# Optimization experiments

Hardware: AMD Instinct MI355X
Metric: run time of the kernel (lower is better)

The kernel has to match this reference:

```python
import jax, jax.numpy as jnp
import numpy as np

EMBED = 1024
HEADS = 16
HEAD_DIM = EMBED // HEADS
HIDDEN = 4096
EPS = 1e-5


def setup_inputs() -> dict:
    key = jax.random.key(0)
    ks = jax.random.split(key, 16)
    s_e = 1.0 / np.sqrt(EMBED)
    s_h = 1.0 / np.sqrt(HIDDEN)
    return {
        "x": jax.random.normal(ks[0], (8, 1024, EMBED), dtype=jnp.float32),
        "ln1_g": jnp.ones((EMBED,), jnp.float32),
        "ln1_b": jnp.zeros((EMBED,), jnp.float32),
        "ln2_g": jnp.ones((EMBED,), jnp.float32),
        "ln2_b": jnp.zeros((EMBED,), jnp.float32),
        "wq": jax.random.uniform(ks[1], (EMBED, EMBED), jnp.float32, -s_e, s_e),
        "bq": jax.random.uniform(ks[2], (EMBED,), jnp.float32, -s_e, s_e),
        "wk": jax.random.uniform(ks[3], (EMBED, EMBED), jnp.float32, -s_e, s_e),
        "bk": jax.random.uniform(ks[4], (EMBED,), jnp.float32, -s_e, s_e),
        "wv": jax.random.uniform(ks[5], (EMBED, EMBED), jnp.float32, -s_e, s_e),
        "bv": jax.random.uniform(ks[6], (EMBED,), jnp.float32, -s_e, s_e),
        "wo": jax.random.uniform(ks[7], (EMBED, EMBED), jnp.float32, -s_e, s_e),
        "bo": jax.random.uniform(ks[8], (EMBED,), jnp.float32, -s_e, s_e),
        "w1": jax.random.uniform(ks[9], (EMBED, HIDDEN), jnp.float32, -s_e, s_e),
        "b1": jax.random.uniform(ks[10], (HIDDEN,), jnp.float32, -s_e, s_e),
        "w2": jax.random.uniform(ks[11], (HIDDEN, EMBED), jnp.float32, -s_h, s_h),
        "b2": jax.random.uniform(ks[12], (EMBED,), jnp.float32, -s_h, s_h),
    }


def _layernorm(x, g, b):
    mu = jnp.mean(x, axis=-1, keepdims=True)
    var = jnp.mean((x - mu) ** 2, axis=-1, keepdims=True)
    return (x - mu) * jax.lax.rsqrt(var + EPS) * g + b


def reference(x, ln1_g, ln1_b, ln2_g, ln2_b, wq, bq, wk, bk, wv, bv, wo, bo, w1, b1, w2, b2):
    B, N, E = x.shape
    scale = HEAD_DIM ** (-0.5)
    # --- attention sublayer (pre-norm) ---
    h = _layernorm(x, ln1_g, ln1_b)
    q = (h @ wq + bq).reshape(B, N, HEADS, HEAD_DIM).transpose(0, 2, 1, 3) * scale
    k = (h @ wk + bk).reshape(B, N, HEADS, HEAD_DIM).transpose(0, 2, 1, 3)
    v = (h @ wv + bv).reshape(B, N, HEADS, HEAD_DIM).transpose(0, 2, 1, 3)
    scores = jnp.einsum("bhqd,bhkd->bhqk", q, k)
    attn = jax.nn.softmax(scores, axis=-1)
    ctx = jnp.einsum("bhqk,bhkd->bhqd", attn, v)
    ctx = ctx.transpose(0, 2, 1, 3).reshape(B, N, E)
    x = x + (ctx @ wo + bo)
    # --- FFN sublayer (pre-norm) ---
    h2 = _layernorm(x, ln2_g, ln2_b)
    ff = jax.nn.relu(h2 @ w1 + b1) @ w2 + b2
    return x + ff
```

## Files before the change

kernel.cpp:

```cpp
#include <hip/hip_runtime.h>
#include <hip/hip_bf16.h>

typedef __attribute__((ext_vector_type(4))) float f32x4;
typedef __attribute__((ext_vector_type(16))) float f32x16;
typedef __attribute__((ext_vector_type(8))) __bf16 bf16x8;
typedef __attribute__((ext_vector_type(4))) __bf16 bf16x4;
typedef __attribute__((ext_vector_type(4))) unsigned int u32x4;

static constexpr int E    = 1024;
static constexpr int TOK  = 8192;
static constexpr int HID  = 4096;

#define DEVINL __device__ __forceinline__

DEVINL void gload16(const void* g, void* l) {
  __builtin_amdgcn_global_load_lds((__attribute__((address_space(1))) void*)g,
                                   (__attribute__((address_space(3))) void*)l, 16, 0, 0);
}

#define ABAR()  asm volatile("s_barrier" ::: "memory")
#define AVM(n)  asm volatile("s_waitcnt vmcnt(" #n ")" ::: "memory")
#define CVTPK(dst, lo, hi) asm("v_cvt_pk_bf16_f32 %0, %1, %2" : "=v"(dst) : "v"(lo), "v"(hi))
#define PLSWAP(a, b) asm("v_permlane32_swap_b32 %0, %1" : "+v"(a), "+v"(b))

__global__ __launch_bounds__(256) void wconv_kernel(const float* __restrict__ W,
                                                    __bf16* __restrict__ Wt,
                                                    int K, int N) {
  __shared__ float tile[32][33];
  const int t  = threadIdx.x;
  const long k0 = (long)blockIdx.y * 32;
  const long n0 = (long)blockIdx.x * 32;
  const int r  = t >> 3;
  const int c4 = (t & 7) * 4;
  float4 v = *(const float4*)&W[(k0 + r) * N + n0 + c4];
  tile[r][c4 + 0] = v.x; tile[r][c4 + 1] = v.y;
  tile[r][c4 + 2] = v.z; tile[r][c4 + 3] = v.w;
  __syncthreads();
  bf16x4 o;
#pragma unroll
  for (int i = 0; i < 4; ++i) o[i] = (__bf16)tile[c4 + i][r];
  *(bf16x4*)&Wt[(n0 + r) * K + k0 + c4] = o;
}

__global__ __launch_bounds__(256) void ln_kernel(const float* __restrict__ X,
                                                 const float* __restrict__ g,
                                                 const float* __restrict__ be,
                                                 __bf16* __restrict__ O) {
  const int t = threadIdx.x;
  const long row = blockIdx.x;
  float4 v = *(const float4*)&X[row * E + t * 4];
  float s  = v.x + v.y + v.z + v.w;
  float ss = v.x * v.x + v.y * v.y + v.z * v.z + v.w * v.w;
#pragma unroll
  for (int off = 32; off; off >>= 1) {
    s  += __shfl_down(s, off);
    ss += __shfl_down(ss, off);
  }
  __shared__ float red[8];
  const int w = t >> 6;
  if ((t & 63) == 0) { red[w] = s; red[4 + w] = ss; }
  __syncthreads();
  s  = red[0] + red[1] + red[2] + red[3];
  ss = red[4] + red[5] + red[6] + red[7];
  const float mean = s * (1.0f / E);
  const float var  = ss * (1.0f / E) - mean * mean;
  const float rstd = rsqrtf(var + 1e-5f);
  float4 gv = *(const float4*)&g[t * 4];
  float4 bv = *(const float4*)&be[t * 4];
  bf16x4 o;
  o[0] = (__bf16)((v.x - mean) * rstd * gv.x + bv.x);
  o[1] = (__bf16)((v.y - mean) * rstd * gv.y + bv.y);
  o[2] = (__bf16)((v.z - mean) * rstd * gv.z + bv.z);
  o[3] = (__bf16)((v.w - mean) * rstd * gv.w + bv.w);
  *(bf16x4*)&O[row * E + t * 4] = o;
}

template <bool RELU, bool RESID, bool OUTBF, int NB>
__global__ __launch_bounds__(512, 2) void gemm8_kernel(const __bf16* __restrict__ A,
                                                       const __bf16* __restrict__ Bt,
                                                       const float* __restrict__ bias0,
                                                       const float* __restrict__ bias1,
                                                       const float* __restrict__ bias2,
                                                       const float* resid,
                                                       void* Cout,
                                                       int M, int N, int K) {
  extern __shared__ char lds[];
  const int tid  = threadIdx.x;
  const int lane = tid & 63;
  const int l15  = lane & 15;
  const int wid  = tid >> 6;
  const int wr   = wid >> 2;
  const int wc   = wid & 3;

  const int nwg  = gridDim.x * gridDim.y;
  const int flat = blockIdx.x + gridDim.x * blockIdx.y;
  const int swz  = (flat & 7) * (nwg >> 3) + (flat >> 3);
  const int bx   = swz % gridDim.x;
  const int by   = swz / gridDim.x;
  const long brow = (long)by * 256;
  const long bcol = (long)bx * 128;

  const __bf16* Ab = A  + brow * K;
  const __bf16* Bb = Bt + bcol * K;
  const int NT = K >> 6;

  char* bA0 = lds;
  char* bA1 = lds + 49152;
  char* bA2 = lds + 98304;

  auto stageA = [&](int k0, char* base, int seg0, int seg1) {
    {
      const int r = seg0 + (tid >> 3);
      const int p = (tid & 7) ^ (r & 7);
      gload16(Ab + (long)r * K + k0 + p * 8, base + seg0 * 128 + tid * 16);
    }
    {
      const int r = seg1 + (tid >> 3);
      const int p = (tid & 7) ^ (r & 7);
      gload16(Ab + (long)r * K + k0 + p * 8, base + seg1 * 128 + tid * 16);
    }
  };
  auto stageB = [&](int k0, char* base) {
#pragma unroll
    for (int i = 0; i < 2; ++i) {
      const int c = i * 64 + (tid >> 3);
      const int p = (tid & 7) ^ (c & 7);
      gload16(Bb + (long)c * K + k0 + p * 8, base + 32768 + i * 8192 + tid * 16);
    }
  };

  f32x4 acc[8][2];
  const f32x4 z4 = {0.f, 0.f, 0.f, 0.f};
#pragma unroll
  for (int m = 0; m < 8; ++m) { acc[m][0] = z4; acc[m][1] = z4; }

  stageA(0, bA0, 0, 128);
  stageA(0, bA0, 64, 192);
  stageB(0, bA0);
  stageA(64, bA1, 0, 128);
  stageA(64, bA1, 64, 192);
  stageB(64, bA1);
  AVM(6);
  ABAR();

  for (int t = 0; t < NT; ++t) {
    const int k2 = (t + 2 < NT) ? ((t + 2) << 6) : 0;

    bf16x8 af[4][2], bfr[2][2];
#pragma unroll
    for (int m = 0; m < 4; ++m)
#pragma unroll
      for (int kk = 0; kk < 2; ++kk) {
        const int row = wr * 128 + m * 16 + l15;
        const int p   = ((kk << 2) + (lane >> 4)) ^ (row & 7);
        af[m][kk] = *(const bf16x8*)(bA0 + row * 128 + p * 16);
      }
#pragma unroll
    for (int n = 0; n < 2; ++n)
#pragma unroll
      for (int kk = 0; kk < 2; ++kk) {
        const int col = wc * 32 + n * 16 + l15;
        const int p   = ((kk << 2) + (lane >> 4)) ^ (col & 7);
        bfr[n][kk] = *(const bf16x8*)(bA0 + 32768 + col * 128 + p * 16);
      }
    stageA(k2, bA2, 0, 128);
    stageB(k2, bA2);
    ABAR();
    __builtin_amdgcn_s_setprio(1);
#pragma unroll
    for (int m = 0; m < 4; ++m)
#pragma unroll
      for (int n = 0; n < 2; ++n) {
        acc[m][n] = __builtin_amdgcn_mfma_f32_16x16x32_bf16(af[m][0], bfr[n][0], acc[m][n], 0, 0, 0);
        acc[m][n] = __builtin_amdgcn_mfma_f32_16x16x32_bf16(af[m][1], bfr[n][1], acc[m][n], 0, 0, 0);
      }
    __builtin_amdgcn_s_setprio(0);
    ABAR();

#pragma unroll
    for (int m = 0; m < 4; ++m)
#pragma unroll
      for (int kk = 0; kk < 2; ++kk) {
        const int row = wr * 128 + (m + 4) * 16 + l15;
        const int p   = ((kk << 2) + (lane >> 4)) ^ (row & 7);
        af[m][kk] = *(const bf16x8*)(bA0 + row * 128 + p * 16);
      }
    stageA(k2, bA2, 64, 192);
    ABAR();
    __builtin_amdgcn_s_setprio(1);
#pragma unroll
    for (int m = 0; m < 4; ++m)
#pragma unroll
      for (int n = 0; n < 2; ++n) {
        acc[m + 4][n] = __builtin_amdgcn_mfma_f32_16x16x32_bf16(af[m][0], bfr[n][0], acc[m + 4][n], 0, 0, 0);
        acc[m + 4][n] = __builtin_amdgcn_mfma_f32_16x16x32_bf16(af[m][1], bfr[n][1], acc[m + 4][n], 0, 0, 0);
      }
    __builtin_amdgcn_s_setprio(0);
    AVM(6);
    ABAR();

    char* tmp = bA0; bA0 = bA1; bA1 = bA2; bA2 = tmp;
  }
  AVM(0);

#pragma unroll
  for (int m = 0; m < 8; ++m) {
#pragma unroll
    for (int n = 0; n < 2; ++n) {
      const long col = bcol + wc * 32 + n * 16 + l15;
      float bb;
      if (NB == 3) {
        const float* bp = (col < 1024) ? bias0 : ((col < 2048) ? bias1 : bias2);
        bb = bp[col & 1023];
      } else {
        bb = bias0[col];
      }
#pragma unroll
      for (int j = 0; j < 4; ++j) {
        const long row = brow + wr * 128 + m * 16 + (lane >> 4) * 4 + j;
        float val = acc[m][n][j] + bb;
        if (RELU) val = fmaxf(val, 0.f);
        const long idx = row * N + col;
        if (RESID) val += resid[idx];
        if (OUTBF) ((__bf16*)Cout)[idx] = (__bf16)val;
        else       ((float*)Cout)[idx]  = val;
      }
    }
  }
}

__global__ __launch_bounds__(256, 3) void attn_kernel(const __bf16* __restrict__ QKV,
                                                      __bf16* __restrict__ Og) {
  __shared__ __align__(16) __bf16 Qs[128 * 64];
  __shared__ __align__(16) __bf16 Ks[2][64 * 64];
  __shared__ __align__(16) __bf16 Vt[2][64 * 64];

  const int QSTR = 3072;
  const int t    = threadIdx.x;
  const int lane = t & 63;
  const int w    = t >> 6;
  const int l31  = lane & 31;
  const int h    = lane >> 5;
  const int b    = blockIdx.y >> 4;
  const int hh   = blockIdx.y & 15;
  const long row0 = (long)b * 1024 + (long)blockIdx.x * 128;
  const long kvrow0 = (long)b * 1024;
  const int colQ = hh * 64;
  const int colK = colQ + 1024;
  const int colV = colQ + 2048;

#pragma unroll
  for (int j = 0; j < 4; ++j) {
    const int c = j * 256 + t;
    const int r = c >> 3;
    const int p = (c & 7) ^ (r & 7);
    gload16(QKV + (row0 + r) * QSTR + colQ + p * 8, (char*)Qs + c * 16);
  }
#pragma unroll
  for (int j = 0; j < 2; ++j) {
    const int c = j * 256 + t;
    const int r = c >> 3;
    const int p = (c & 7) ^ (r & 7);
    gload16(QKV + (kvrow0 + r) * QSTR + colK + p * 8, (char*)Ks[0] + c * 16);
  }
  bf16x8 vv[2];
#pragma unroll
  for (int j = 0; j < 2; ++j) {
    const int c = j * 256 + t;
    const int key = c >> 3, dc = c & 7;
    vv[j] = *(const bf16x8*)(QKV + (kvrow0 + key) * QSTR + colV + dc * 8);
  }
  AVM(0);
#pragma unroll
  for (int j = 0; j < 2; ++j) {
    const int c = j * 256 + t;
    const int key = c >> 3, dc = c & 7;
#pragma unroll
    for (int e = 0; e < 8; ++e) {
      const int d = dc * 8 + e;
      *(__bf16*)((char*)Vt[0] + d * 128 + (((key >> 3) ^ dc) * 16) + (key & 7) * 2) = vv[j][e];
    }
  }
  __syncthreads();

  bf16x8 bq[4];
  {
    const int qrow = w * 32 + l31;
#pragma unroll
    for (int kk = 0; kk < 4; ++kk) {
      const int p = (kk * 2 + h) ^ (qrow & 7);
      bq[kk] = *(const bf16x8*)((const char*)Qs + qrow * 128 + p * 16);
    }
  }

  f32x16 ctx0, ctx1;
#pragma unroll
  for (int r = 0; r < 16; ++r) { ctx0[r] = 0.f; ctx1[r] = 0.f; }
  float m = -INFINITY, l = 0.f;

  for (int kb = 0; kb < 16; ++kb) {
    const int cur = kb & 1, nxt = cur ^ 1;
    const int kb1 = (kb + 1 < 16) ? kb + 1 : kb;
    const long kr1 = kvrow0 + kb1 * 64;

#pragma unroll
    for (int j = 0; j < 2; ++j) {
      const int c = j * 256 + t;
      const int key = c >> 3, dc = c & 7;
      vv[j] = *(const bf16x8*)(QKV + (kr1 + key) * QSTR + colV + dc * 8);
    }
#pragma unroll
    for (int j = 0; j < 2; ++j) {
      const int c = j * 256 + t;
      const int r = c >> 3;
      const int p = (c & 7) ^ (r & 7);
      gload16(QKV + (kr1 + r) * QSTR + colK + p * 8, (char*)Ks[nxt] + c * 16);
    }

    f32x16 s0, s1;
#pragma unroll
    for (int r = 0; r < 16; ++r) { s0[r] = 0.f; s1[r] = 0.f; }
    __builtin_amdgcn_s_setprio(1);
#pragma unroll
    for (int kk = 0; kk < 4; ++kk) {
      const int pce = kk * 2 + h;
      const int p0i = pce ^ (l31 & 7);
      bf16x8 ak0 = *(const bf16x8*)((const char*)Ks[cur] + l31 * 128 + p0i * 16);
      bf16x8 ak1 = *(const bf16x8*)((const char*)Ks[cur] + (32 + l31) * 128 + p0i * 16);
      s0 = __builtin_amdgcn_mfma_f32_32x32x16_bf16(ak0, bq[kk], s0, 0, 0, 0);
      s1 = __builtin_amdgcn_mfma_f32_32x32x16_bf16(ak1, bq[kk], s1, 0, 0, 0);
    }
    __builtin_amdgcn_s_setprio(0);

    float mx = s0[0];
#pragma unroll
    for (int r = 1; r < 16; ++r) mx = fmaxf(mx, s0[r]);
#pragma unroll
    for (int r = 0; r < 16; ++r) mx = fmaxf(mx, s1[r]);
    mx = fmaxf(mx, __shfl_xor(mx, 32));

    if (!__all(mx - m <= 64.f)) {
      const float mn = fmaxf(m, mx);
      const float corr = __expf((m - mn) * 0.125f);
      l *= corr;
#pragma unroll
      for (int r = 0; r < 16; ++r) { ctx0[r] *= corr; ctx1[r] *= corr; }
      m = mn;
    }
    f32x16 p0, p1;
    float rs = 0.f;
#pragma unroll
    for (int r = 0; r < 16; ++r) { p0[r] = __expf((s0[r] - m) * 0.125f); rs += p0[r]; }
#pragma unroll
    for (int r = 0; r < 16; ++r) { p1[r] = __expf((s1[r] - m) * 0.125f); rs += p1[r]; }
    rs += __shfl_xor(rs, 32);
    l += rs;

    AVM(2);
#pragma unroll
    for (int j = 0; j < 2; ++j) {
      const int c = j * 256 + t;
      const int key = c >> 3, dc = c & 7;
#pragma unroll
      for (int e = 0; e < 8; ++e) {
        const int d = dc * 8 + e;
        *(__bf16*)((char*)Vt[nxt] + d * 128 + (((key >> 3) ^ dc) * 16) + (key & 7) * 2) = vv[j][e];
      }
    }

    bf16x8 paf[4];
#pragma unroll
    for (int ks = 0; ks < 4; ++ks) {
      const int base = (ks & 1) * 8;
      unsigned a0, a1, b0, b1;
      if (ks < 2) {
        CVTPK(a0, p0[base + 0], p0[base + 1]);
        CVTPK(b0, p0[base + 4], p0[base + 5]);
        CVTPK(a1, p0[base + 2], p0[base + 3]);
        CVTPK(b1, p0[base + 6], p0[base + 7]);
      } else {
        CVTPK(a0, p1[base + 0], p1[base + 1]);
        CVTPK(b0, p1[base + 4], p1[base + 5]);
        CVTPK(a1, p1[base + 2], p1[base + 3]);
        CVTPK(b1, p1[base + 6], p1[base + 7]);
      }
      PLSWAP(a0, b0);
      PLSWAP(a1, b1);
      u32x4 wv4; wv4[0] = a0; wv4[1] = a1; wv4[2] = b0; wv4[3] = b1;
      paf[ks] = __builtin_bit_cast(bf16x8, wv4);
    }

    __builtin_amdgcn_s_setprio(1);
#pragma unroll
    for (int ks = 0; ks < 4; ++ks) {
      const int pce = ks * 2 + h;
      bf16x8 av0 = *(const bf16x8*)((const char*)Vt[cur] + l31 * 128 + ((pce ^ (l31 >> 3)) * 16));
      bf16x8 av1 = *(const bf16x8*)((const char*)Vt[cur] + (32 + l31) * 128 + ((pce ^ (4 + (l31 >> 3))) * 16));
      ctx0 = __builtin_amdgcn_mfma_f32_32x32x16_bf16(av0, paf[ks], ctx0, 0, 0, 0);
      ctx1 = __builtin_amdgcn_mfma_f32_32x32x16_bf16(av1, paf[ks], ctx1, 0, 0, 0);
    }
    __builtin_amdgcn_s_setprio(0);

    __syncthreads();
  }

  const float inv = 1.0f / l;
  const long orow = row0 + w * 32 + l31;
#pragma unroll
  for (int f = 0; f < 2; ++f)
#pragma unroll
    for (int tq = 0; tq < 4; ++tq) {
      bf16x4 o;
#pragma unroll
      for (int e = 0; e < 4; ++e) {
        const float v = (f ? ctx1[tq * 4 + e] : ctx0[tq * 4 + e]) * inv;
        o[e] = (__bf16)v;
      }
      const int col = colQ + f * 32 + tq * 8 + h * 4;
      *(bf16x4*)&Og[orow * E + col] = o;
    }
}

extern "C" void kernel_launch(void* const* d_in, const int* in_sizes, int n_in,
                              void* d_out, int out_size, void* d_ws, size_t ws_size,
                              hipStream_t stream) {
  const float* x     = (const float*)d_in[0];
  const float* ln1g  = (const float*)d_in[1];
  const float* ln1b  = (const float*)d_in[2];
  const float* ln2g  = (const float*)d_in[3];
  const float* ln2b  = (const float*)d_in[4];
  const float* wq    = (const float*)d_in[5];
  const float* bq    = (const float*)d_in[6];
  const float* wk    = (const float*)d_in[7];
  const float* bk    = (const float*)d_in[8];
  const float* wv    = (const float*)d_in[9];
  const float* bv    = (const float*)d_in[10];
  const float* wo    = (const float*)d_in[11];
  const float* bo    = (const float*)d_in[12];
  const float* w1    = (const float*)d_in[13];
  const float* b1    = (const float*)d_in[14];
  const float* w2    = (const float*)d_in[15];
  const float* b2    = (const float*)d_in[16];
  float* out = (float*)d_out;

  char* ws = (char*)d_ws;
  const size_t MB = 1024 * 1024;
  __bf16* Wqkv = (__bf16*)(ws + 0 * MB);
  __bf16* Wot  = (__bf16*)(ws + 6 * MB);
  __bf16* W1t  = (__bf16*)(ws + 8 * MB);
  __bf16* W2t  = (__bf16*)(ws + 16 * MB);
  __bf16* h    = (__bf16*)(ws + 24 * MB);
  __bf16* qkv  = (__bf16*)(ws + 40 * MB);
  __bf16* ctx  = (__bf16*)(ws + 88 * MB);
  __bf16* ff1  = (__bf16*)(ws + 40 * MB);

  const dim3 blk(256);
  const dim3 blk512(512);
  const size_t GLDS = 147456;

  wconv_kernel<<<dim3(E / 32, E / 32), blk, 0, stream>>>(wq, Wqkv, E, E);
  wconv_kernel<<<dim3(E / 32, E / 32), blk, 0, stream>>>(wk, Wqkv + 1024 * 1024, E, E);
  wconv_kernel<<<dim3(E / 32, E / 32), blk, 0, stream>>>(wv, Wqkv + 2048 * 1024, E, E);
  wconv_kernel<<<dim3(E / 32, E / 32), blk, 0, stream>>>(wo, Wot, E, E);
  wconv_kernel<<<dim3(HID / 32, E / 32), blk, 0, stream>>>(w1, W1t, E, HID);
  wconv_kernel<<<dim3(E / 32, HID / 32), blk, 0, stream>>>(w2, W2t, HID, E);

  ln_kernel<<<TOK, blk, 0, stream>>>(x, ln1g, ln1b, h);

  gemm8_kernel<false, false, true, 3><<<dim3(3072 / 128, TOK / 256), blk512, GLDS, stream>>>(
      h, Wqkv, bq, bk, bv, nullptr, qkv, TOK, 3072, E);

  attn_kernel<<<dim3(8, 128), blk, 0, stream>>>(qkv, ctx);

  gemm8_kernel<false, true, false, 1><<<dim3(E / 128, TOK / 256), blk512, GLDS, stream>>>(
      ctx, Wot, bo, nullptr, nullptr, x, out, TOK, E, E);

  ln_kernel<<<TOK, blk, 0, stream>>>(out, ln2g, ln2b, h);

  gemm8_kernel<true, false, true, 1><<<dim3(HID / 128, TOK / 256), blk512, GLDS, stream>>>(
      h, W1t, b1, nullptr, nullptr, nullptr, ff1, TOK, HID, E);

  gemm8_kernel<false, true, false, 1><<<dim3(E / 128, TOK / 256), blk512, GLDS, stream>>>(
      ff1, W2t, b2, nullptr, nullptr, out, out, TOK, E, HID);
}
```

Baseline: 371.3 us.

## Widen GEMM tiles to 256 columns with double-buffered split-phase pipeline

Replaces the 256x128 triple-buffered GEMM with a templated kernel whose tiles are 256x256 (QKV, FFN1) or 128x256 (out-proj, FFN2). It double-buffers LDS and issues half-tile loads interleaved with four MFMA quadrants per k-step. The aim is more data reuse per loaded byte and lower LDS footprint per block. In exchange it doubles the accumulator registers for the 256x256 case, which could lower occupancy or cause spills, and the narrower grids on the N=1024 GEMMs give fewer blocks.

Measured after the change: 353.5 us. -4.8%, faster.

```diff
diff --git a/kernel.cpp b/kernel.cpp
--- a/kernel.cpp
+++ b/kernel.cpp
@@ -22,6 +22,14 @@
 #define AVM(n)  asm volatile("s_waitcnt vmcnt(" #n ")" ::: "memory")
 #define CVTPK(dst, lo, hi) asm("v_cvt_pk_bf16_f32 %0, %1, %2" : "=v"(dst) : "v"(lo), "v"(hi))
 #define PLSWAP(a, b) asm("v_permlane32_swap_b32 %0, %1" : "+v"(a), "+v"(b))
+
+template <int N> DEVINL void avm() {
+  if constexpr (N == 0)      asm volatile("s_waitcnt vmcnt(0)" ::: "memory");
+  else if constexpr (N == 2) asm volatile("s_waitcnt vmcnt(2)" ::: "memory");
+  else if constexpr (N == 3) asm volatile("s_waitcnt vmcnt(3)" ::: "memory");
+  else if constexpr (N == 4) asm volatile("s_waitcnt vmcnt(4)" ::: "memory");
+  else                       asm volatile("s_waitcnt vmcnt(6)" ::: "memory");
+}
 
 __global__ __launch_bounds__(256) void wconv_kernel(const float* __restrict__ W,
                                                     __bf16* __restrict__ Wt,
@@ -75,16 +83,23 @@
   *(bf16x4*)&O[row * E + t * 4] = o;
 }
 
-template <bool RELU, bool RESID, bool OUTBF, int NB>
-__global__ __launch_bounds__(512, 2) void gemm8_kernel(const __bf16* __restrict__ A,
-                                                       const __bf16* __restrict__ Bt,
-                                                       const float* __restrict__ bias0,
-                                                       const float* __restrict__ bias1,
-                                                       const float* __restrict__ bias2,
-                                                       const float* resid,
-                                                       void* Cout,
-                                                       int M, int N, int K) {
+template <int BM_, bool RELU, bool RESID, bool OUTBF, int NB>
+__global__ __launch_bounds__(512, 2) void gemm256_kernel(const __bf16* __restrict__ A,
+                                                         const __bf16* __restrict__ Bt,
+                                                         const float* __restrict__ bias0,
+                                                         const float* __restrict__ bias1,
+                                                         const float* __restrict__ bias2,
+                                                         const float* resid,
+                                                         void* Cout,
+                                                         int M, int N, int K) {
   extern __shared__ char lds[];
+  constexpr int MH   = BM_ / 64;
+  constexpr int ASZ  = BM_ * 128;
+  constexpr int BOFF = 2 * ASZ;
+  constexpr int V1   = (BM_ == 256) ? 4 : 3;
+  constexpr int V2   = (BM_ == 256) ? 4 : 2;
+  constexpr int V3   = (BM_ == 256) ? 4 : 3;
+
   const int tid  = threadIdx.x;
   const int lane = tid & 63;
   const int l15  = lane & 15;
@@ -97,117 +112,115 @@
   const int swz  = (flat & 7) * (nwg >> 3) + (flat >> 3);
   const int bx   = swz % gridDim.x;
   const int by   = swz / gridDim.x;
-  const long brow = (long)by * 256;
-  const long bcol = (long)bx * 128;
+  const long brow = (long)by * BM_;
+  const long bcol = (long)bx * 256;
 
   const __bf16* Ab = A  + brow * K;
   const __bf16* Bb = Bt + bcol * K;
   const int NT = K >> 6;
 
-  char* bA0 = lds;
-  char* bA1 = lds + 49152;
-  char* bA2 = lds + 98304;
-
-  auto stageA = [&](int k0, char* base, int seg0, int seg1) {
-    {
-      const int r = seg0 + (tid >> 3);
-      const int p = (tid & 7) ^ (r & 7);
-      gload16(Ab + (long)r * K + k0 + p * 8, base + seg0 * 128 + tid * 16);
-    }
-    {
-      const int r = seg1 + (tid >> 3);
-      const int p = (tid & 7) ^ (r & 7);
-      gload16(Ab + (long)r * K + k0 + p * 8, base + seg1 * 128 + tid * 16);
+  auto stageAhalf = [&](int k0, int rbase, char* dst) {
+#pragma unroll
+    for (int i = 0; i < BM_ / 128; ++i) {
+      const int c = i * 512 + tid;
+      const int r = c >> 3;
+      const int p = (c & 7) ^ (r & 7);
+      gload16(Ab + (long)(rbase + r) * K + k0 + p * 8, dst + c * 16);
     }
   };
-  auto stageB = [&](int k0, char* base) {
+  auto stageBhalf = [&](int k0, int cbase, char* dst) {
 #pragma unroll
     for (int i = 0; i < 2; ++i) {
-      const int c = i * 64 + (tid >> 3);
-      const int p = (tid & 7) ^ (c & 7);
-      gload16(Bb + (long)c * K + k0 + p * 8, base + 32768 + i * 8192 + tid * 16);
+      const int c = i * 512 + tid;
+      const int r = c >> 3;
+      const int p = (c & 7) ^ (r & 7);
+      gload16(Bb + (long)(cbase + r) * K + k0 + p * 8, dst + c * 16);
     }
   };
 
-  f32x4 acc[8][2];
+  f32x4 acc[2 * MH][4];
   const f32x4 z4 = {0.f, 0.f, 0.f, 0.f};
 #pragma unroll
-  for (int m = 0; m < 8; ++m) { acc[m][0] = z4; acc[m][1] = z4; }
-
-  stageA(0, bA0, 0, 128);
-  stageA(0, bA0, 64, 192);
-  stageB(0, bA0);
-  stageA(64, bA1, 0, 128);
-  stageA(64, bA1, 64, 192);
-  stageB(64, bA1);
-  AVM(6);
-  ABAR();
+  for (int m = 0; m < 2 * MH; ++m)
+#pragma unroll
+    for (int n = 0; n < 4; ++n) acc[m][n] = z4;
+
+  bf16x8 af[MH][2], bfr[4][2];
+
+  auto readA = [&](const char* Ac, int mbase) {
+#pragma unroll
+    for (int mm = 0; mm < MH; ++mm)
+#pragma unroll
+      for (int kk = 0; kk < 2; ++kk) {
+        const int row = (mbase + mm) * 32 + wr * 16 + l15;
+        const int p   = ((kk << 2) + (lane >> 4)) ^ (row & 7);
+        af[mm][kk] = *(const bf16x8*)(Ac + row * 128 + p * 16);
+      }
+  };
+  auto readB = [&](const char* Bc, int nbase) {
+#pragma unroll
+    for (int nn = 0; nn < 2; ++nn)
+#pragma unroll
+      for (int kk = 0; kk < 2; ++kk) {
+        const int col = (nbase + nn) * 64 + wc * 16 + l15;
+        const int p   = ((kk << 2) + (lane >> 4)) ^ (col & 7);
+        bfr[nbase + nn][kk] = *(const bf16x8*)(Bc + col * 128 + p * 16);
+      }
+  };
+  auto domfma = [&](int mb, int nb) {
+    __builtin_amdgcn_s_setprio(1);
+#pragma unroll
+    for (int mm = 0; mm < MH; ++mm)
+#pragma unroll
+      for (int nn = 0; nn < 2; ++nn) {
+        f32x4 a = acc[mb + mm][nb + nn];
+        a = __builtin_amdgcn_mfma_f32_16x16x32_bf16(af[mm][0], bfr[nb + nn][0], a, 0, 0, 0);
+        a = __builtin_amdgcn_mfma_f32_16x16x32_bf16(af[mm][1], bfr[nb + nn][1], a, 0, 0, 0);
+        acc[mb + mm][nb + nn] = a;
+      }
+    __builtin_amdgcn_s_setprio(0);
+  };
+
+  stageAhalf(0, 0, lds);
+  stageBhalf(0, 0, lds + BOFF);
+  stageBhalf(0, 128, lds + BOFF + 16384);
+  stageAhalf(0, BM_ / 2, lds + ASZ / 2);
 
   for (int t = 0; t < NT; ++t) {
-    const int k2 = (t + 2 < NT) ? ((t + 2) << 6) : 0;
-
-    bf16x8 af[4][2], bfr[2][2];
-#pragma unroll
-    for (int m = 0; m < 4; ++m)
-#pragma unroll
-      for (int kk = 0; kk < 2; ++kk) {
-        const int row = wr * 128 + m * 16 + l15;
-        const int p   = ((kk << 2) + (lane >> 4)) ^ (row & 7);
-        af[m][kk] = *(const bf16x8*)(bA0 + row * 128 + p * 16);
-      }
-#pragma unroll
-    for (int n = 0; n < 2; ++n)
-#pragma unroll
-      for (int kk = 0; kk < 2; ++kk) {
-        const int col = wc * 32 + n * 16 + l15;
-        const int p   = ((kk << 2) + (lane >> 4)) ^ (col & 7);
-        bfr[n][kk] = *(const bf16x8*)(bA0 + 32768 + col * 128 + p * 16);
-      }
-    stageA(k2, bA2, 0, 128);
-    stageB(k2, bA2);
-    ABAR();
-    __builtin_amdgcn_s_setprio(1);
-#pragma unroll
-    for (int m = 0; m < 4; ++m)
-#pragma unroll
-      for (int n = 0; n < 2; ++n) {
-        acc[m][n] = __builtin_amdgcn_mfma_f32_16x16x32_bf16(af[m][0], bfr[n][0], acc[m][n], 0, 0, 0);
-        acc[m][n] = __builtin_amdgcn_mfma_f32_16x16x32_bf16(af[m][1], bfr[n][1], acc[m][n], 0, 0, 0);
-      }
-    __builtin_amdgcn_s_setprio(0);
-    ABAR();
-
-#pragma unroll
-    for (int m = 0; m < 4; ++m)
-#pragma unroll
-      for (int kk = 0; kk < 2; ++kk) {
-        const int row = wr * 128 + (m + 4) * 16 + l15;
-        const int p   = ((kk << 2) + (lane >> 4)) ^ (row & 7);
-        af[m][kk] = *(const bf16x8*)(bA0 + row * 128 + p * 16);
-      }
-    stageA(k2, bA2, 64, 192);
-    ABAR();
-    __builtin_amdgcn_s_setprio(1);
-#pragma unroll
-    for (int m = 0; m < 4; ++m)
-#pragma unroll
-      for (int n = 0; n < 2; ++n) {
-        acc[m + 4][n] = __builtin_amdgcn_mfma_f32_16x16x32_bf16(af[m][0], bfr[n][0], acc[m + 4][n], 0, 0, 0);
-        acc[m + 4][n] = __builtin_amdgcn_mfma_f32_16x16x32_bf16(af[m][1], bfr[n][1], acc[m + 4][n], 0, 0, 0);
-      }
-    __builtin_amdgcn_s_setprio(0);
-    AVM(6);
-    ABAR();
-
-    char* tmp = bA0; bA0 = bA1; bA1 = bA2; bA2 = tmp;
-  }
-  AVM(0);
-
-#pragma unroll
-  for (int m = 0; m < 8; ++m) {
-#pragma unroll
-    for (int n = 0; n < 2; ++n) {
-      const long col = bcol + wc * 32 + n * 16 + l15;
+    const int cur = t & 1;
+    const int nxt = cur ^ 1;
+    char* Ac = lds + cur * ASZ;
+    char* Bc = lds + BOFF + cur * 32768;
+    char* An = lds + nxt * ASZ;
+    char* Bn = lds + BOFF + nxt * 32768;
+    const int kt = (t + 1 < NT) ? ((t + 1) << 6) : 0;
+
+    avm<V1>(); ABAR();
+    readA(Ac, 0);
+    readB(Bc, 0);
+    stageAhalf(kt, 0, An);
+    domfma(0, 0);
+
+    avm<V2>(); ABAR();
+    readB(Bc, 2);
+    stageBhalf(kt, 0, Bn);
+    domfma(0, 2);
+
+    avm<V3>(); ABAR();
+    readA(Ac, MH);
+    stageBhalf(kt, 128, Bn + 16384);
+    domfma(MH, 0);
+
+    stageAhalf(kt, BM_ / 2, An + ASZ / 2);
+    domfma(MH, 2);
+  }
+  avm<0>();
+
+#pragma unroll
+  for (int m = 0; m < 2 * MH; ++m) {
+#pragma unroll
+    for (int n = 0; n < 4; ++n) {
+      const long col = bcol + n * 64 + wc * 16 + l15;
       float bb;
       if (NB == 3) {
         const float* bp = (col < 1024) ? bias0 : ((col < 2048) ? bias1 : bias2);
@@ -217,7 +230,7 @@
       }
 #pragma unroll
       for (int j = 0; j < 4; ++j) {
-        const long row = brow + wr * 128 + m * 16 + (lane >> 4) * 4 + j;
+        const long row = brow + m * 32 + wr * 16 + (lane >> 4) * 4 + j;
         float val = acc[m][n][j] + bb;
         if (RELU) val = fmaxf(val, 0.f);
         const long idx = row * N + col;
@@ -456,7 +469,8 @@
 
   const dim3 blk(256);
   const dim3 blk512(512);
-  const size_t GLDS = 147456;
+  const size_t GLDS256 = 131072;
+  const size_t GLDS128 = 98304;
 
   wconv_kernel<<<dim3(E / 32, E / 32), blk, 0, stream>>>(wq, Wqkv, E, E);
   wconv_kernel<<<dim3(E / 32, E / 32), blk, 0, stream>>>(wk, Wqkv + 1024 * 1024, E, E);
@@ -467,19 +481,19 @@
 
   ln_kernel<<<TOK, blk, 0, stream>>>(x, ln1g, ln1b, h);
 
-  gemm8_kernel<false, false, true, 3><<<dim3(3072 / 128, TOK / 256), blk512, GLDS, stream>>>(
+  gemm256_kernel<256, false, false, true, 3><<<dim3(3072 / 256, TOK / 256), blk512, GLDS256, stream>>>(
       h, Wqkv, bq, bk, bv, nullptr, qkv, TOK, 3072, E);
 
   attn_kernel<<<dim3(8, 128), blk, 0, stream>>>(qkv, ctx);
 
-  gemm8_kernel<false, true, false, 1><<<dim3(E / 128, TOK / 256), blk512, GLDS, stream>>>(
+  gemm256_kernel<128, false, true, false, 1><<<dim3(E / 256, TOK / 128), blk512, GLDS128, stream>>>(
       ctx, Wot, bo, nullptr, nullptr, x, out, TOK, E, E);
 
   ln_kernel<<<TOK, blk, 0, stream>>>(out, ln2g, ln2b, h);
 
-  gemm8_kernel<true, false, true, 1><<<dim3(HID / 128, TOK / 256), blk512, GLDS, stream>>>(
+  gemm256_kernel<256, true, false, true, 1><<<dim3(HID / 256, TOK / 256), blk512, GLDS256, stream>>>(
       h, W1t, b1, nullptr, nullptr, nullptr, ff1, TOK, HID, E);
 
-  gemm8_kernel<false, true, false, 1><<<dim3(E / 128, TOK / 256), blk512, GLDS, stream>>>(
+  gemm256_kernel<128, false, true, false, 1><<<dim3(E / 256, TOK / 128), blk512, GLDS128, stream>>>(
       ff1, W2t, b2, nullptr, nullptr, out, out, TOK, E, HID);
 }
```

## Rework GEMM to BK=32 deep multi-stage pipeline with templated tile shapes

Applied to the files above, without the earlier changes.

Replaces the fixed 256x128 triple-buffered BK=64 GEMM with a templated kernel that uses 256-wide N tiles, BK=32 K-steps and a configurable pipeline depth (4 stages for BM=256, 5 for BM=128), with a new XOR swizzle and interleaved wave layout. The narrow-N projections (Wo and W2) switch to 128x256 tiles to keep enough workgroups in flight. The aim is to hide global-load latency better and raise MFMA reuse per LDS read. In exchange there is one barrier per K-step instead of several, a different LDS footprint that may change occupancy, and per-stage waitcnt values that are hand-derived.

After: 367.1 us. Within noise of the previous version (-1.2%).

```diff
diff --git a/kernel.cpp b/kernel.cpp
--- a/kernel.cpp
+++ b/kernel.cpp
@@ -22,6 +22,14 @@
 #define AVM(n)  asm volatile("s_waitcnt vmcnt(" #n ")" ::: "memory")
 #define CVTPK(dst, lo, hi) asm("v_cvt_pk_bf16_f32 %0, %1, %2" : "=v"(dst) : "v"(lo), "v"(hi))
 #define PLSWAP(a, b) asm("v_permlane32_swap_b32 %0, %1" : "+v"(a), "+v"(b))
+
+template <int N> DEVINL void avm() {
+  if constexpr (N == 0)      asm volatile("s_waitcnt vmcnt(0)" ::: "memory");
+  else if constexpr (N == 2) asm volatile("s_waitcnt vmcnt(2)" ::: "memory");
+  else if constexpr (N == 8) asm volatile("s_waitcnt vmcnt(8)" ::: "memory");
+  else if constexpr (N == 9) asm volatile("s_waitcnt vmcnt(9)" ::: "memory");
+  else                       asm volatile("s_waitcnt vmcnt(0)" ::: "memory");
+}
 
 __global__ __launch_bounds__(256) void wconv_kernel(const float* __restrict__ W,
                                                     __bf16* __restrict__ Wt,
@@ -75,8 +83,8 @@
   *(bf16x4*)&O[row * E + t * 4] = o;
 }
 
-template <bool RELU, bool RESID, bool OUTBF, int NB>
-__global__ __launch_bounds__(512, 2) void gemm8_kernel(const __bf16* __restrict__ A,
+template <int BM_, int DEPTH, bool RELU, bool RESID, bool OUTBF, int NB>
+__global__ __launch_bounds__(512, 2) void gemmk_kernel(const __bf16* __restrict__ A,
                                                        const __bf16* __restrict__ Bt,
                                                        const float* __restrict__ bias0,
                                                        const float* __restrict__ bias1,
@@ -85,9 +93,17 @@
                                                        void* Cout,
                                                        int M, int N, int K) {
   extern __shared__ char lds[];
+  constexpr int MF    = BM_ / 32;
+  constexpr int ABYT  = BM_ * 64;
+  constexpr int TILEB = ABYT + 16384;
+  constexpr int AL    = BM_ / 128;
+  constexpr int TL    = AL + 2;
+  constexpr int W     = (DEPTH - 2) * TL;
+
   const int tid  = threadIdx.x;
   const int lane = tid & 63;
   const int l15  = lane & 15;
+  const int kp   = lane >> 4;
   const int wid  = tid >> 6;
   const int wr   = wid >> 2;
   const int wc   = wid & 3;
@@ -97,117 +113,119 @@
   const int swz  = (flat & 7) * (nwg >> 3) + (flat >> 3);
   const int bx   = swz % gridDim.x;
   const int by   = swz / gridDim.x;
-  const long brow = (long)by * 256;
-  const long bcol = (long)bx * 128;
+  const long brow = (long)by * BM_;
+  const long bcol = (long)bx * 256;
 
   const __bf16* Ab = A  + brow * K;
   const __bf16* Bb = Bt + bcol * K;
-  const int NT = K >> 6;
-
-  char* bA0 = lds;
-  char* bA1 = lds + 49152;
-  char* bA2 = lds + 98304;
-
-  auto stageA = [&](int k0, char* base, int seg0, int seg1) {
-    {
-      const int r = seg0 + (tid >> 3);
-      const int p = (tid & 7) ^ (r & 7);
-      gload16(Ab + (long)r * K + k0 + p * 8, base + seg0 * 128 + tid * 16);
-    }
-    {
-      const int r = seg1 + (tid >> 3);
-      const int p = (tid & 7) ^ (r & 7);
-      gload16(Ab + (long)r * K + k0 + p * 8, base + seg1 * 128 + tid * 16);
+  const int NT = K >> 5;
+
+  auto stageA = [&](int k0, char* dst) {
+#pragma unroll
+    for (int i = 0; i < AL; ++i) {
+      const int c = i * 512 + tid;
+      const int r = c >> 2;
+      const int p = (c & 3) ^ ((r >> 1) & 3);
+      gload16(Ab + (long)r * K + k0 + p * 8, dst + c * 16);
     }
   };
-  auto stageB = [&](int k0, char* base) {
+  auto stageB = [&](int k0, char* dst) {
 #pragma unroll
     for (int i = 0; i < 2; ++i) {
-      const int c = i * 64 + (tid >> 3);
-      const int p = (tid & 7) ^ (c & 7);
-      gload16(Bb + (long)c * K + k0 + p * 8, base + 32768 + i * 8192 + tid * 16);
+      const int c = i * 512 + tid;
+      const int r = c >> 2;
+      const int p = (c & 3) ^ ((r >> 1) & 3);
+      gload16(Bb + (long)r * K + k0 + p * 8, dst + c * 16);
     }
   };
 
-  f32x4 acc[8][2];
+  f32x4 acc[MF][4];
   const f32x4 z4 = {0.f, 0.f, 0.f, 0.f};
 #pragma unroll
-  for (int m = 0; m < 8; ++m) { acc[m][0] = z4; acc[m][1] = z4; }
-
-  stageA(0, bA0, 0, 128);
-  stageA(0, bA0, 64, 192);
-  stageB(0, bA0);
-  stageA(64, bA1, 0, 128);
-  stageA(64, bA1, 64, 192);
-  stageB(64, bA1);
-  AVM(6);
-  ABAR();
+  for (int m = 0; m < MF; ++m)
+#pragma unroll
+    for (int n = 0; n < 4; ++n) acc[m][n] = z4;
+
+#pragma unroll
+  for (int pt = 0; pt < DEPTH - 1; ++pt) {
+    stageA(pt * 32, lds + pt * TILEB);
+    stageB(pt * 32, lds + pt * TILEB + ABYT);
+  }
+
+  bf16x8 af[MF > 4 ? 4 : MF], bfr[4];
 
   for (int t = 0; t < NT; ++t) {
-    const int k2 = (t + 2 < NT) ? ((t + 2) << 6) : 0;
-
-    bf16x8 af[4][2], bfr[2][2];
-#pragma unroll
-    for (int m = 0; m < 4; ++m)
-#pragma unroll
-      for (int kk = 0; kk < 2; ++kk) {
-        const int row = wr * 128 + m * 16 + l15;
-        const int p   = ((kk << 2) + (lane >> 4)) ^ (row & 7);
-        af[m][kk] = *(const bf16x8*)(bA0 + row * 128 + p * 16);
-      }
-#pragma unroll
-    for (int n = 0; n < 2; ++n)
-#pragma unroll
-      for (int kk = 0; kk < 2; ++kk) {
-        const int col = wc * 32 + n * 16 + l15;
-        const int p   = ((kk << 2) + (lane >> 4)) ^ (col & 7);
-        bfr[n][kk] = *(const bf16x8*)(bA0 + 32768 + col * 128 + p * 16);
-      }
-    stageA(k2, bA2, 0, 128);
-    stageB(k2, bA2);
+    const int cb = t % DEPTH;
+    const int sb = (t + DEPTH - 1) % DEPTH;
+    const char* Ac = lds + cb * TILEB;
+    const char* Bc = Ac + ABYT;
+    char* An = lds + sb * TILEB;
+    const int kt = (t + DEPTH - 1 < NT) ? ((t + DEPTH - 1) << 5) : 0;
+
+    avm<W>();
     ABAR();
-    __builtin_amdgcn_s_setprio(1);
-#pragma unroll
-    for (int m = 0; m < 4; ++m)
-#pragma unroll
-      for (int n = 0; n < 2; ++n) {
-        acc[m][n] = __builtin_amdgcn_mfma_f32_16x16x32_bf16(af[m][0], bfr[n][0], acc[m][n], 0, 0, 0);
-        acc[m][n] = __builtin_amdgcn_mfma_f32_16x16x32_bf16(af[m][1], bfr[n][1], acc[m][n], 0, 0, 0);
-      }
-    __builtin_amdgcn_s_setprio(0);
-    ABAR();
-
-#pragma unroll
-    for (int m = 0; m < 4; ++m)
-#pragma unroll
-      for (int kk = 0; kk < 2; ++kk) {
-        const int row = wr * 128 + (m + 4) * 16 + l15;
-        const int p   = ((kk << 2) + (lane >> 4)) ^ (row & 7);
-        af[m][kk] = *(const bf16x8*)(bA0 + row * 128 + p * 16);
-      }
-    stageA(k2, bA2, 64, 192);
-    ABAR();
-    __builtin_amdgcn_s_setprio(1);
-#pragma unroll
-    for (int m = 0; m < 4; ++m)
-#pragma unroll
-      for (int n = 0; n < 2; ++n) {
-        acc[m + 4][n] = __builtin_amdgcn_mfma_f32_16x16x32_bf16(af[m][0], bfr[n][0], acc[m + 4][n], 0, 0, 0);
-        acc[m + 4][n] = __builtin_amdgcn_mfma_f32_16x16x32_bf16(af[m][1], bfr[n][1], acc[m + 4][n], 0, 0, 0);
-      }
-    __builtin_amdgcn_s_setprio(0);
-    AVM(6);
-    ABAR();
-
-    char* tmp = bA0; bA0 = bA1; bA1 = bA2; bA2 = tmp;
-  }
-  AVM(0);
-
-#pragma unroll
-  for (int m = 0; m < 8; ++m) {
-#pragma unroll
-    for (int n = 0; n < 2; ++n) {
-      const long col = bcol + wc * 32 + n * 16 + l15;
+
+    if constexpr (BM_ == 256) {
+#pragma unroll
+      for (int m = 0; m < 4; ++m) {
+        const int row = m * 32 + wr * 16 + l15;
+        af[m] = *(const bf16x8*)(Ac + row * 64 + (kp ^ ((row >> 1) & 3)) * 16);
+      }
+#pragma unroll
+      for (int n = 0; n < 4; ++n) {
+        const int col = n * 64 + wc * 16 + l15;
+        bfr[n] = *(const bf16x8*)(Bc + col * 64 + (kp ^ ((col >> 1) & 3)) * 16);
+      }
+      stageA(kt, An);
+      __builtin_amdgcn_s_setprio(1);
+#pragma unroll
+      for (int m = 0; m < 4; ++m)
+#pragma unroll
+        for (int n = 0; n < 4; ++n)
+          acc[m][n] = __builtin_amdgcn_mfma_f32_16x16x32_bf16(af[m], bfr[n], acc[m][n], 0, 0, 0);
+      __builtin_amdgcn_s_setprio(0);
+#pragma unroll
+      for (int m = 0; m < 4; ++m) {
+        const int row = (m + 4) * 32 + wr * 16 + l15;
+        af[m] = *(const bf16x8*)(Ac + row * 64 + (kp ^ ((row >> 1) & 3)) * 16);
+      }
+      stageB(kt, An + ABYT);
+      __builtin_amdgcn_s_setprio(1);
+#pragma unroll
+      for (int m = 0; m < 4; ++m)
+#pragma unroll
+        for (int n = 0; n < 4; ++n)
+          acc[m + 4][n] = __builtin_amdgcn_mfma_f32_16x16x32_bf16(af[m], bfr[n], acc[m + 4][n], 0, 0, 0);
+      __builtin_amdgcn_s_setprio(0);
+    } else {
+#pragma unroll
+      for (int m = 0; m < 4; ++m) {
+        const int row = m * 32 + wr * 16 + l15;
+        af[m] = *(const bf16x8*)(Ac + row * 64 + (kp ^ ((row >> 1) & 3)) * 16);
+      }
+#pragma unroll
+      for (int n = 0; n < 4; ++n) {
+        const int col = n * 64 + wc * 16 + l15;
+        bfr[n] = *(const bf16x8*)(Bc + col * 64 + (kp ^ ((col >> 1) & 3)) * 16);
+      }
+      stageA(kt, An);
+      stageB(kt, An + ABYT);
+      __builtin_amdgcn_s_setprio(1);
+#pragma unroll
+      for (int m = 0; m < 4; ++m)
+#pragma unroll
+        for (int n = 0; n < 4; ++n)
+          acc[m][n] = __builtin_amdgcn_mfma_f32_16x16x32_bf16(af[m], bfr[n], acc[m][n], 0, 0, 0);
+      __builtin_amdgcn_s_setprio(0);
+    }
+  }
+  avm<0>();
+
+#pragma unroll
+  for (int m = 0; m < MF; ++m) {
+#pragma unroll
+    for (int n = 0; n < 4; ++n) {
+      const long col = bcol + n * 64 + wc * 16 + l15;
       float bb;
       if (NB == 3) {
         const float* bp = (col < 1024) ? bias0 : ((col < 2048) ? bias1 : bias2);
@@ -217,7 +235,7 @@
       }
 #pragma unroll
       for (int j = 0; j < 4; ++j) {
-        const long row = brow + wr * 128 + m * 16 + (lane >> 4) * 4 + j;
+        const long row = brow + m * 32 + wr * 16 + (lane >> 4) * 4 + j;
         float val = acc[m][n][j] + bb;
         if (RELU) val = fmaxf(val, 0.f);
         const long idx = row * N + col;
@@ -456,7 +474,8 @@
 
   const dim3 blk(256);
   const dim3 blk512(512);
-  const size_t GLDS = 147456;
+  const size_t GLDS256 = 4 * (256 * 64 + 16384);
+  const size_t GLDS128 = 5 * (128 * 64 + 16384);
 
   wconv_kernel<<<dim3(E / 32, E / 32), blk, 0, stream>>>(wq, Wqkv, E, E);
   wconv_kernel<<<dim3(E / 32, E / 32), blk, 0, stream>>>(wk, Wqkv + 1024 * 1024, E, E);
@@ -467,19 +486,19 @@
 
   ln_kernel<<<TOK, blk, 0, stream>>>(x, ln1g, ln1b, h);
 
-  gemm8_kernel<false, false, true, 3><<<dim3(3072 / 128, TOK / 256), blk512, GLDS, stream>>>(
+  gemmk_kernel<256, 4, false, false, true, 3><<<dim3(3072 / 256, TOK / 256), blk512, GLDS256, stream>>>(
       h, Wqkv, bq, bk, bv, nullptr, qkv, TOK, 3072, E);
 
   attn_kernel<<<dim3(8, 128), blk, 0, stream>>>(qkv, ctx);
 
-  gemm8_kernel<false, true, false, 1><<<dim3(E / 128, TOK / 256), blk512, GLDS, stream>>>(
+  gemmk_kernel<128, 5, false, true, false, 1><<<dim3(E / 256, TOK / 128), blk512, GLDS128, stream>>>(
       ctx, Wot, bo, nullptr, nullptr, x, out, TOK, E, E);
 
   ln_kernel<<<TOK, blk, 0, stream>>>(out, ln2g, ln2b, h);
 
-  gemm8_kernel<true, false, true, 1><<<dim3(HID / 128, TOK / 256), blk512, GLDS, stream>>>(
+  gemmk_kernel<256, 4, true, false, true, 1><<<dim3(HID / 256, TOK / 256), blk512, GLDS256, stream>>>(
       h, W1t, b1, nullptr, nullptr, nullptr, ff1, TOK, HID, E);
 
-  gemm8_kernel<false, true, false, 1><<<dim3(E / 128, TOK / 256), blk512, GLDS, stream>>>(
+  gemmk_kernel<128, 5, false, true, false, 1><<<dim3(E / 256, TOK / 128), blk512, GLDS128, stream>>>(
       ff1, W2t, b2, nullptr, nullptr, out, out, TOK, E, HID);
 }
```
